# Kernel optimization log

Hardware: AMD Instinct MI355X
Metric: run time of the kernel (lower is better)

## Reference

```python
import jax, jax.numpy as jnp
import numpy as np

B, DIM, HEADS, HW = 32, 384, 8, 48
CH = DIM // HEADS  # 48 channels per head


def pool_matrix(H, s):
    # PyTorch AdaptiveAvgPool2d binning: start=floor(i*H/s), end=ceil((i+1)*H/s)
    P = np.zeros((s, H), np.float32)
    for i in range(s):
        a = (i * H) // s
        b = -((-(i + 1) * H) // s)
        P[i, a:b] = 1.0 / (b - a)
    return jnp.asarray(P)


def dwconv(x, w, b, p):
    # depthwise conv, NCHW, kernel [C,1,k,k], stride 1, symmetric pad p
    y = jax.lax.conv_general_dilated(
        x, w, (1, 1), [(p, p), (p, p)],
        dimension_numbers=('NCHW', 'OIHW', 'NCHW'),
        feature_group_count=x.shape[1])
    if b is not None:
        y = y + b[None, :, None, None]
    return y


def setup_inputs() -> dict:
    key = jax.random.key(0)
    ks = jax.random.split(key, 10)
    s = 0.02
    return {
        'x': jax.random.normal(ks[0], (B, DIM, HW, HW), jnp.float32),
        'ln_w': jnp.ones((DIM,), jnp.float32),
        'ln_b': jnp.zeros((DIM,), jnp.float32),
        'w_qkv': jax.random.normal(ks[1], (3 * DIM, DIM), jnp.float32) * s,
        'w_dw': jax.random.normal(ks[2], (3 * DIM, 1, 3, 3), jnp.float32) * s,
        'temperature': jnp.ones((HEADS, 1, 1), jnp.float32),
        'conv3_w': jax.random.normal(ks[3], (3 * CH, 1, 3, 3), jnp.float32) * s,
        'conv3_b': jnp.zeros((3 * CH,), jnp.float32),
        'conv5_w': jax.random.normal(ks[4], (3 * CH, 1, 5, 5), jnp.float32) * s,
        'conv5_b': jnp.zeros((3 * CH,), jnp.float32),
        'conv7_w': jax.random.normal(ks[5], (2 * CH, 1, 7, 7), jnp.float32) * s,
        'conv7_b': jnp.zeros((2 * CH,), jnp.float32),
        'w_proj': jax.random.normal(ks[6], (DIM, DIM), jnp.float32) * s,
    }


def reference(x, ln_w, ln_b, w_qkv, w_dw, temperature,
              conv3_w, conv3_b, conv5_w, conv5_b, conv7_w, conv7_b, w_proj):
    b, C, H, W = x.shape
    heads, Ch = HEADS, C // HEADS
    N = H * W
    # WithBias LayerNorm over channel dim (biased variance, eps 1e-5)
    mu = x.mean(axis=1, keepdims=True)
    var = ((x - mu) ** 2).mean(axis=1, keepdims=True)
    xn = (x - mu) / jnp.sqrt(var + 1e-5) * ln_w[None, :, None, None] + ln_b[None, :, None, None]
    # qkv: 1x1 conv then depthwise 3x3 (groups = 3*dim)
    qkv = jnp.einsum('bchw,oc->bohw', xn, w_qkv)
    qkv = dwconv(qkv, w_dw, None, 1)
    q, k, v = jnp.split(qkv, 3, axis=1)
    q = q.reshape(b, heads, Ch, N)
    k = k.reshape(b, heads, Ch, N)
    v = v.reshape(b, heads, Ch, N)
    # L2-normalize along token dim (F.normalize eps=1e-12)
    qn = q / jnp.maximum(jnp.linalg.norm(q, axis=-1, keepdims=True), 1e-12)
    kn = k / jnp.maximum(jnp.linalg.norm(k, axis=-1, keepdims=True), 1e-12)
    # channel attention [b,h,Ch,Ch]
    attn = jax.nn.relu(jnp.einsum('bhcn,bhdn->bhcd', qn, kn) * temperature[None])
    # ---- FilterModule (crpe) ----
    v_img = v.reshape(b, heads * Ch, H, W)
    # low-pass: 4 equal channel chunks, adaptive avg pool to (1,3,5,7), bilinear up
    chunk = (heads * Ch) // 4
    lp_parts = []
    for idx, sz in enumerate((1, 3, 5, 7)):
        part = v_img[:, idx * chunk:(idx + 1) * chunk]
        Pr = pool_matrix(H, sz)
        Pc = pool_matrix(W, sz)
        pooled = jnp.einsum('ph,bchw,qw->bcpq', Pr, part, Pc)
        lp_parts.append(jax.image.resize(pooled, (b, chunk, H, W), method='linear'))
    LP = jax.nn.relu(jnp.concatenate(lp_parts, axis=1))
    # high-pass: grouped depthwise convs on [3Ch, 3Ch, 2Ch] channel splits
    s0, s1 = 3 * Ch, 3 * Ch
    HP = jnp.concatenate([
        dwconv(v_img[:, :s0], conv3_w, conv3_b, 1),
        dwconv(v_img[:, s0:s0 + s1], conv5_w, conv5_b, 2),
        dwconv(v_img[:, s0 + s1:], conv7_w, conv7_b, 3),
    ], axis=1)
    HP = HP.reshape(b, heads, Ch, N)
    LPf = LP.reshape(b, heads, Ch, N)
    crpe = qn * HP + LPf
    # ---- output ----
    out = jnp.einsum('bhcd,bhdn->bhcn', attn, v)
    out = (Ch ** -0.5) * out + crpe
    out = out.reshape(b, C, H, W)
    out = jnp.einsum('bchw,oc->bohw', out, w_proj)
    return out
```

## Files before the change

kernel.cpp:

```cpp
#include <hip/hip_runtime.h>

typedef unsigned short u16;
typedef short sh4 __attribute__((ext_vector_type(4)));
typedef short short8 __attribute__((ext_vector_type(8)));
typedef u16 ush8 __attribute__((ext_vector_type(8)));
typedef __bf16 bf16x8 __attribute__((ext_vector_type(8)));
typedef float f32x4 __attribute__((ext_vector_type(4)));

#define NB 32
#define CDIM 384
#define NSP 2304
#define QCH 1152

__device__ __forceinline__ float b2f(u16 u) {
    union { unsigned i; float f; } v; v.i = ((unsigned)u) << 16; return v.f;
}
__device__ __forceinline__ u16 f2b(float f) {
    union { float f; unsigned i; } v; v.f = f;
    unsigned r = v.i + 0x7FFFu + ((v.i >> 16) & 1u);
    return (u16)(r >> 16);
}

__global__ __launch_bounds__(256) void k_prep(const float* __restrict__ wqkv,
                                              const float* __restrict__ wproj,
                                              u16* __restrict__ wqkv_bf,
                                              u16* __restrict__ wproj_bf) {
    int i = blockIdx.x * 256 + threadIdx.x;
    if (i < QCH * CDIM) wqkv_bf[i] = f2b(wqkv[i]);
    if (i < CDIM * CDIM) wproj_bf[i] = f2b(wproj[i]);
}

__global__ __launch_bounds__(256) void k_ln(const float* __restrict__ x,
                                            const float* __restrict__ lnw,
                                            const float* __restrict__ lnb,
                                            u16* __restrict__ xnt) {
    __shared__ float s_sum[4][64], s_sq[4][64], s_mu[64], s_rs[64];
    __shared__ u16 s_tile[64][392];
    int b = blockIdx.y, n0 = blockIdx.x * 64;
    int tid = threadIdx.x, c4 = tid >> 6, nl = tid & 63;
    int cbase = c4 * 96;
    const float* xb = x + (size_t)b * CDIM * NSP + (size_t)cbase * NSP + n0 + nl;
    float v[96];
    float sum = 0.f, sq = 0.f;
#pragma unroll
    for (int j = 0; j < 96; j++) {
        v[j] = xb[(size_t)j * NSP];
        sum += v[j]; sq += v[j] * v[j];
    }
    s_sum[c4][nl] = sum; s_sq[c4][nl] = sq;
    __syncthreads();
    if (tid < 64) {
        float s = s_sum[0][tid] + s_sum[1][tid] + s_sum[2][tid] + s_sum[3][tid];
        float q = s_sq[0][tid] + s_sq[1][tid] + s_sq[2][tid] + s_sq[3][tid];
        float mu = s * (1.f / CDIM);
        float var = q * (1.f / CDIM) - mu * mu;
        s_mu[tid] = mu; s_rs[tid] = rsqrtf(var + 1e-5f);
    }
    __syncthreads();
    float mu = s_mu[nl], rs = s_rs[nl];
#pragma unroll
    for (int j = 0; j < 96; j++) {
        int c = cbase + j;
        s_tile[nl][c] = f2b((v[j] - mu) * rs * lnw[c] + lnb[c]);
    }
    __syncthreads();
    u16* o = xnt + ((size_t)b * NSP + n0) * CDIM;
    for (int i = tid; i < 64 * 48; i += 256) {
        int row = i / 48, c8 = i % 48;
        *(short8*)(o + row * CDIM + c8 * 8) = *(const short8*)(&s_tile[row][c8 * 8]);
    }
}

__global__ __launch_bounds__(256) void k_gemm(const u16* __restrict__ A,
                                              const u16* __restrict__ Bt,
                                              void* __restrict__ Cmat, int M, int f32out) {
    __shared__ u16 As[128][40], Bs[128][40];
    int tid = threadIdx.x;
    int bxn = blockIdx.x, bym = blockIdx.y, bz = blockIdx.z;
    int wave = tid >> 6, lane = tid & 63, wr = wave >> 1, wc = wave & 1;
    int lr = lane & 15, lk = lane >> 4;
    f32x4 acc[4][4];
#pragma unroll
    for (int m = 0; m < 4; m++)
#pragma unroll
        for (int n = 0; n < 4; n++) acc[m][n] = (f32x4){0.f, 0.f, 0.f, 0.f};
    int rs = tid >> 2, ks = (tid & 3) * 8;
    const u16* Ap0 = A + (size_t)(bym * 128 + rs) * 384 + ks;
    const u16* Ap1 = Ap0 + (size_t)64 * 384;
    const u16* Bp0 = Bt + ((size_t)bz * NSP + bxn * 128 + rs) * 384 + ks;
    const u16* Bp1 = Bp0 + (size_t)64 * 384;
    for (int k0 = 0; k0 < 384; k0 += 32) {
        *(short8*)(&As[rs][ks])      = *(const short8*)(Ap0 + k0);
        *(short8*)(&As[rs + 64][ks]) = *(const short8*)(Ap1 + k0);
        *(short8*)(&Bs[rs][ks])      = *(const short8*)(Bp0 + k0);
        *(short8*)(&Bs[rs + 64][ks]) = *(const short8*)(Bp1 + k0);
        __syncthreads();
        short8 af[4], bfr[4];
#pragma unroll
        for (int m = 0; m < 4; m++) af[m] = *(const short8*)(&As[wr * 64 + m * 16 + lr][lk * 8]);
#pragma unroll
        for (int n = 0; n < 4; n++) bfr[n] = *(const short8*)(&Bs[wc * 64 + n * 16 + lr][lk * 8]);
#pragma unroll
        for (int m = 0; m < 4; m++)
#pragma unroll
            for (int n = 0; n < 4; n++)
                acc[m][n] = __builtin_amdgcn_mfma_f32_16x16x32_bf16(
                    __builtin_bit_cast(bf16x8, af[m]), __builtin_bit_cast(bf16x8, bfr[n]),
                    acc[m][n], 0, 0, 0);
        __syncthreads();
    }
#pragma unroll
    for (int m = 0; m < 4; m++)
#pragma unroll
        for (int n = 0; n < 4; n++) {
            int row = bym * 128 + wr * 64 + m * 16 + lk * 4;
            int col = bxn * 128 + wc * 64 + n * 16 + lr;
            if (f32out) {
                float* cp = (float*)Cmat + ((size_t)bz * M + row) * NSP + col;
#pragma unroll
                for (int r = 0; r < 4; r++) cp[(size_t)r * NSP] = acc[m][n][r];
            } else {
                u16* cp = (u16*)Cmat + ((size_t)bz * M + row) * NSP + col;
#pragma unroll
                for (int r = 0; r < 4; r++) cp[(size_t)r * NSP] = f2b(acc[m][n][r]);
            }
        }
}

__global__ __launch_bounds__(192) void k_dw3(u16* __restrict__ qkv,
                                             const float* __restrict__ wdw,
                                             float* __restrict__ sumsq) {
    __shared__ u16 s_in[4 * 2304];
    __shared__ float s_part[192];
    int bx = blockIdx.x, b = blockIdx.y, tid = threadIdx.x;
    u16* gbase = qkv + ((size_t)b * QCH + bx * 4) * NSP;
#pragma unroll
    for (int i = 0; i < 6; i++) {
        int c = tid + i * 192;
        *(ush8*)(&s_in[c * 8]) = *(const ush8*)(gbase + c * 8);
    }
    int p = tid / 48, y = tid % 48;
    int ch = bx * 4 + p;
    float w[9];
#pragma unroll
    for (int i = 0; i < 9; i++) w[i] = wdw[ch * 9 + i];
    __syncthreads();
    const u16* L = &s_in[p * 2304];
    ush8 r0[6], r1[6], r2[6];
#pragma unroll
    for (int o = 0; o < 6; o++) {
        r1[o] = *(const ush8*)(L + y * 48 + o * 8);
        if (y > 0)  r0[o] = *(const ush8*)(L + (y - 1) * 48 + o * 8); else r0[o] = 0;
        if (y < 47) r2[o] = *(const ush8*)(L + (y + 1) * 48 + o * 8); else r2[o] = 0;
    }
    float ss = 0.f;
    short8 outv[6];
#pragma unroll
    for (int g = 0; g < 6; g++) {
        float a0[10], a1[10], a2[10];
#pragma unroll
        for (int j = 0; j < 10; j++) {
            int xi = g * 8 - 1 + j;
            if (xi < 0 || xi >= 48) { a0[j] = 0.f; a1[j] = 0.f; a2[j] = 0.f; }
            else {
                a0[j] = b2f(r0[xi >> 3][xi & 7]);
                a1[j] = b2f(r1[xi >> 3][xi & 7]);
                a2[j] = b2f(r2[xi >> 3][xi & 7]);
            }
        }
        union { u16 u[8]; short8 v; } pk;
#pragma unroll
        for (int x = 0; x < 8; x++) {
            float o = a0[x] * w[0] + a0[x + 1] * w[1] + a0[x + 2] * w[2]
                    + a1[x] * w[3] + a1[x + 1] * w[4] + a1[x + 2] * w[5]
                    + a2[x] * w[6] + a2[x + 1] * w[7] + a2[x + 2] * w[8];
            ss += o * o;
            pk.u[x] = f2b(o);
        }
        outv[g] = pk.v;
    }
    s_part[tid] = ss;
    __syncthreads();
#pragma unroll
    for (int g = 0; g < 6; g++)
        *(short8*)(&s_in[p * 2304 + y * 48 + g * 8]) = outv[g];
    __syncthreads();
#pragma unroll
    for (int i = 0; i < 6; i++) {
        int c = tid + i * 192;
        *(ush8*)(gbase + c * 8) = *(const ush8*)(&s_in[c * 8]);
    }
    if (bx < 192 && tid < 4) {
        float s = 0.f;
        for (int i = 0; i < 48; i++) s += s_part[tid * 48 + i];
        sumsq[b * 768 + bx * 4 + tid] = s;
    }
}

__global__ void k_rnorm(const float* __restrict__ ss, float* __restrict__ rn) {
    int i = blockIdx.x * 256 + threadIdx.x;
    if (i < NB * 768) rn[i] = 1.f / fmaxf(sqrtf(ss[i]), 1e-12f);
}

__global__ __launch_bounds__(512) void k_attn(const u16* __restrict__ qkv,
                                              const float* __restrict__ rn,
                                              const float* __restrict__ temp,
                                              u16* __restrict__ attn) {
    __shared__ float s_part[8][48 * 48];
    int h = blockIdx.x, b = blockIdx.y, tid = threadIdx.x;
    int wave = tid >> 6, lane = tid & 63;
    int lr = lane & 15, lk = lane >> 4;
    const u16* qp = qkv + ((size_t)b * QCH + h * 48) * NSP;
    const u16* kp = qkv + ((size_t)b * QCH + 384 + h * 48) * NSP;
    f32x4 acc[3][3];
#pragma unroll
    for (int m = 0; m < 3; m++)
#pragma unroll
        for (int n = 0; n < 3; n++) acc[m][n] = (f32x4){0.f, 0.f, 0.f, 0.f};
    int k0 = wave * 288 + lk * 8;
    short8 af[3], bf[3], afn[3], bfn[3];
#pragma unroll
    for (int m = 0; m < 3; m++) {
        af[m] = *(const short8*)(qp + (size_t)(m * 16 + lr) * NSP + k0);
        bf[m] = *(const short8*)(kp + (size_t)(m * 16 + lr) * NSP + k0);
    }
    for (int s = 0; s < 9; s++) {
        if (s < 8) {
#pragma unroll
            for (int m = 0; m < 3; m++) {
                afn[m] = *(const short8*)(qp + (size_t)(m * 16 + lr) * NSP + k0 + 32 * (s + 1));
                bfn[m] = *(const short8*)(kp + (size_t)(m * 16 + lr) * NSP + k0 + 32 * (s + 1));
            }
        }
#pragma unroll
        for (int m = 0; m < 3; m++)
#pragma unroll
            for (int n = 0; n < 3; n++)
                acc[m][n] = __builtin_amdgcn_mfma_f32_16x16x32_bf16(
                    __builtin_bit_cast(bf16x8, af[m]), __builtin_bit_cast(bf16x8, bf[n]),
                    acc[m][n], 0, 0, 0);
#pragma unroll
        for (int m = 0; m < 3; m++) { af[m] = afn[m]; bf[m] = bfn[m]; }
    }
#pragma unroll
    for (int m = 0; m < 3; m++)
#pragma unroll
        for (int n = 0; n < 3; n++)
#pragma unroll
            for (int r = 0; r < 4; r++)
                s_part[wave][(m * 16 + lk * 4 + r) * 48 + n * 16 + lr] = acc[m][n][r];
    __syncthreads();
    float th = temp[h];
    const float* rq = rn + b * 768 + h * 48;
    const float* rk = rn + b * 768 + 384 + h * 48;
    u16* ap = attn + ((size_t)(b * 8 + h)) * NSP;
    for (int f = tid; f < 2304; f += 512) {
        int c = f / 48, d = f % 48;
        float v = 0.f;
#pragma unroll
        for (int wv = 0; wv < 8; wv++) v += s_part[wv][f];
        v *= th * rq[c] * rk[d];
        ap[f] = f2b(fmaxf(v, 0.f));
    }
}

template<int KS, int CH0, int NCH>
__global__ __launch_bounds__(256) void k_hp_t(const u16* __restrict__ qkv,
                                              const float* __restrict__ wk,
                                              const float* __restrict__ bk,
                                              u16* __restrict__ hp) {
    constexpr int PAD = KS / 2;
    constexpr int NIN = 8 + 2 * PAD;
    int t = blockIdx.x * 256 + threadIdx.x;
    int y = t % 48;
    int rem = t / 48;
    int chl = rem % NCH;
    int b = rem / NCH;
    int ch = CH0 + chl;
    const u16* src = qkv + ((size_t)b * QCH + 768 + ch) * NSP;
    float bias = bk[chl];
    float acc[48];
#pragma unroll
    for (int i = 0; i < 48; i++) acc[i] = bias;
    for (int dy = 0; dy < KS; dy++) {
        int yy = y - PAD + dy;
        if (yy < 0 || yy >= 48) continue;
        ush8 r[6];
#pragma unroll
        for (int o = 0; o < 6; o++) r[o] = *(const ush8*)(src + yy * 48 + o * 8);
        float wr[KS];
#pragma unroll
        for (int dx = 0; dx < KS; dx++) wr[dx] = wk[chl * KS * KS + dy * KS + dx];
#pragma unroll
        for (int g = 0; g < 6; g++) {
            float a[NIN];
#pragma unroll
            for (int j = 0; j < NIN; j++) {
                int xi = g * 8 - PAD + j;
                a[j] = (xi < 0 || xi >= 48) ? 0.f : b2f(r[xi >> 3][xi & 7]);
            }
#pragma unroll
            for (int x = 0; x < 8; x++) {
                float s = 0.f;
#pragma unroll
                for (int dx = 0; dx < KS; dx++) s += a[x + dx] * wr[dx];
                acc[g * 8 + x] += s;
            }
        }
    }
    u16* dst = hp + ((size_t)b * CDIM + ch) * NSP + y * 48;
#pragma unroll
    for (int g = 0; g < 6; g++) {
        union { u16 u[8]; short8 v; } pk;
#pragma unroll
        for (int x = 0; x < 8; x++) pk.u[x] = f2b(acc[g * 8 + x]);
        *(short8*)(dst + g * 8) = pk.v;
    }
}

__global__ __launch_bounds__(64) void k_pool(const u16* __restrict__ qkv,
                                             float* __restrict__ pooled) {
    int c = blockIdx.x, b = blockIdx.y, tid = threadIdx.x;
    int s = 2 * (c / 96) + 1;
    __shared__ u16 s_p[2304];
    __shared__ float rp[48][7];
    const u16* src = qkv + ((size_t)b * QCH + 768 + c) * NSP;
    for (int f = tid; f < 288; f += 64)
        *(ush8*)(&s_p[f * 8]) = *(const ush8*)(src + f * 8);
    __syncthreads();
    if (tid < 48) {
        for (int q = 0; q < s; q++) {
            int a = q * 48 / s, e = ((q + 1) * 48 + s - 1) / s;
            float sum = 0.f;
            for (int xx = a; xx < e; xx++) sum += b2f(s_p[tid * 48 + xx]);
            rp[tid][q] = sum / (float)(e - a);
        }
    }
    __syncthreads();
    if (tid < s * s) {
        int p = tid / s, q = tid % s;
        int a = p * 48 / s, e = ((p + 1) * 48 + s - 1) / s;
        float sum = 0.f;
        for (int r = a; r < e; r++) sum += rp[r][q];
        pooled[((size_t)b * CDIM + c) * 49 + tid] = sum / (float)(e - a);
    }
}

__global__ __launch_bounds__(256) void k_out(const u16* __restrict__ qkv,
                                             const u16* __restrict__ attn,
                                             const float* __restrict__ rn,
                                             const u16* __restrict__ hp,
                                             const float* __restrict__ pooled,
                                             u16* __restrict__ tmpt) {
    int nc = blockIdx.x, h = blockIdx.y, b = blockIdx.z, tid = threadIdx.x;
    __shared__ u16 s_at[48 * 72];
    __shared__ u16 s_vt[64 * 72];
    __shared__ float s_pool[48][49];
    __shared__ float s_rq[48];
    int n0 = nc * 64;
    for (int f = tid; f < 432; f += 256) *(ush8*)(&s_at[f * 8]) = (ush8)0;
    for (int f = tid; f < 576; f += 256) *(ush8*)(&s_vt[f * 8]) = (ush8)0;
    __syncthreads();
    const u16* ag = attn + ((size_t)(b * 8 + h)) * NSP;
    for (int f = tid; f < 288; f += 256) {
        int c = f / 6, j = f % 6;
        *(ush8*)(&s_at[c * 72 + j * 8]) = *(const ush8*)(ag + c * 48 + j * 8);
    }
    const u16* vsrc = qkv + ((size_t)b * QCH + 768 + h * 48) * NSP + n0;
    for (int f = tid; f < 3072; f += 256) {
        int d = f >> 6, nn = f & 63;
        s_vt[nn * 72 + d] = vsrc[(size_t)d * NSP + nn];
    }
    for (int f = tid; f < 48 * 49; f += 256)
        s_pool[f / 49][f % 49] = pooled[((size_t)b * CDIM + h * 48) * 49 + f];
    if (tid < 48) s_rq[tid] = rn[b * 768 + h * 48 + tid];
    __syncthreads();
    int wave = tid >> 6, lane = tid & 63, lr = lane & 15, lk = lane >> 4;
    f32x4 acc[3];
#pragma unroll
    for (int m = 0; m < 3; m++) acc[m] = (f32x4){0.f, 0.f, 0.f, 0.f};
#pragma unroll
    for (int ks = 0; ks < 2; ks++) {
        short8 bfr = *(const short8*)(&s_vt[(wave * 16 + lr) * 72 + ks * 32 + lk * 8]);
#pragma unroll
        for (int m = 0; m < 3; m++) {
            short8 af = *(const short8*)(&s_at[(m * 16 + lr) * 72 + ks * 32 + lk * 8]);
            acc[m] = __builtin_amdgcn_mfma_f32_16x16x32_bf16(
                __builtin_bit_cast(bf16x8, af), __builtin_bit_cast(bf16x8, bfr),
                acc[m], 0, 0, 0);
        }
    }
    int s = 2 * (h / 2) + 1;
    const float inv = 0.14433756729740643f;
    int n = n0 + wave * 16 + lr;
    int y = n / 48, xx = n % 48;
    float syf = (y + 0.5f) * s * (1.f / 48.f) - 0.5f;
    int iy0 = (int)floorf(syf); float fy = syf - (float)iy0;
    int iy1 = min(iy0 + 1, s - 1); iy0 = max(iy0, 0);
    float sxf = (xx + 0.5f) * s * (1.f / 48.f) - 0.5f;
    int ix0 = (int)floorf(sxf); float fx = sxf - (float)ix0;
    int ix1 = min(ix0 + 1, s - 1); ix0 = max(ix0, 0);
    const u16* qp = qkv + ((size_t)b * QCH + h * 48) * NSP + n;
    const u16* hq = hp + ((size_t)b * CDIM + h * 48) * NSP + n;
    u16* tp = tmpt + ((size_t)b * NSP + n) * CDIM + h * 48;
#pragma unroll
    for (int m = 0; m < 3; m++) {
        int cb = m * 16 + lk * 4;
        union { u16 u[4]; sh4 v; } pk;
#pragma unroll
        for (int r = 0; r < 4; r++) {
            int ch = cb + r;
            float qv = b2f(qp[(size_t)ch * NSP]);
            float hv = b2f(hq[(size_t)ch * NSP]);
            const float* P = s_pool[ch];
            float lp = (1.f - fy) * ((1.f - fx) * P[iy0 * s + ix0] + fx * P[iy0 * s + ix1])
                     + fy * ((1.f - fx) * P[iy1 * s + ix0] + fx * P[iy1 * s + ix1]);
            lp = fmaxf(lp, 0.f);
            pk.u[r] = f2b(inv * acc[m][r] + qv * s_rq[ch] * hv + lp);
        }
        *(sh4*)(tp + cb) = pk.v;
    }
}

extern "C" void kernel_launch(void* const* d_in, const int* in_sizes, int n_in,
                              void* d_out, int out_size, void* d_ws, size_t ws_size,
                              hipStream_t stream) {
    const float* x    = (const float*)d_in[0];
    const float* lnw  = (const float*)d_in[1];
    const float* lnb  = (const float*)d_in[2];
    const float* wqkv = (const float*)d_in[3];
    const float* wdw  = (const float*)d_in[4];
    const float* temp = (const float*)d_in[5];
    const float* w3   = (const float*)d_in[6];
    const float* b3   = (const float*)d_in[7];
    const float* w5   = (const float*)d_in[8];
    const float* b5   = (const float*)d_in[9];
    const float* w7   = (const float*)d_in[10];
    const float* b7   = (const float*)d_in[11];
    const float* wproj= (const float*)d_in[12];
    float* out = (float*)d_out;

    char* w = (char*)d_ws;
    const size_t SZ_XNT = (size_t)NB * NSP * CDIM * 2;
    const size_t SZ_QKV = (size_t)NB * QCH * NSP * 2;
    u16* xnt      = (u16*)w;
    u16* qkvb     = (u16*)(w + SZ_XNT);
    u16* hpb      = (u16*)(w + SZ_XNT + SZ_QKV);
    char* tail    = w + SZ_XNT + SZ_QKV + (size_t)NB * CDIM * NSP * 2;
    float* sumsq  = (float*)tail;
    float* rnorm  = sumsq + NB * 768;
    u16*  attnb   = (u16*)(rnorm + NB * 768);
    float* pooled = (float*)(attnb + (size_t)NB * 8 * NSP);
    u16* wqkv_bf  = (u16*)(pooled + (size_t)NB * CDIM * 49);
    u16* wproj_bf = wqkv_bf + (size_t)QCH * CDIM;
    u16* tmpt = xnt;

    k_prep <<<dim3((QCH * CDIM + 255) / 256), 256, 0, stream>>>(wqkv, wproj, wqkv_bf, wproj_bf);
    k_ln   <<<dim3(36, NB), 256, 0, stream>>>(x, lnw, lnb, xnt);
    k_gemm <<<dim3(18, 9, NB), 256, 0, stream>>>(wqkv_bf, xnt, qkvb, QCH, 0);
    k_dw3  <<<dim3(288, NB), 192, 0, stream>>>(qkvb, wdw, sumsq);
    k_rnorm<<<dim3(96), 256, 0, stream>>>(sumsq, rnorm);
    k_attn <<<dim3(8, NB), 512, 0, stream>>>(qkvb, rnorm, temp, attnb);
    k_hp_t<3, 0, 144>   <<<dim3(864), 256, 0, stream>>>(qkvb, w3, b3, hpb);
    k_hp_t<5, 144, 144> <<<dim3(864), 256, 0, stream>>>(qkvb, w5, b5, hpb);
    k_hp_t<7, 288, 96>  <<<dim3(576), 256, 0, stream>>>(qkvb, w7, b7, hpb);
    k_pool <<<dim3(CDIM, NB), 64, 0, stream>>>(qkvb, pooled);
    k_out  <<<dim3(36, 8, NB), 256, 0, stream>>>(qkvb, attnb, rnorm, hpb, pooled, tmpt);
    k_gemm <<<dim3(18, 3, NB), 256, 0, stream>>>(wproj_bf, tmpt, out, CDIM, 1);
}
```

Baseline: 466.7 us.

## Load GEMM tiles via direct global-to-LDS loads with XOR swizzle and BK=64

```diff
diff --git a/kernel.cpp b/kernel.cpp
--- a/kernel.cpp
+++ b/kernel.cpp
@@ -19,6 +19,10 @@
     union { float f; unsigned i; } v; v.f = f;
     unsigned r = v.i + 0x7FFFu + ((v.i >> 16) & 1u);
     return (u16)(r >> 16);
+}
+__device__ __forceinline__ void gload16(const u16* g, u16* l) {
+    __builtin_amdgcn_global_load_lds((const __attribute__((address_space(1))) unsigned int*)(g),
+                                     (__attribute__((address_space(3))) unsigned int*)(l), 16, 0, 0);
 }
 
 __global__ __launch_bounds__(256) void k_prep(const float* __restrict__ wqkv,
@@ -74,7 +78,8 @@
 __global__ __launch_bounds__(256) void k_gemm(const u16* __restrict__ A,
                                               const u16* __restrict__ Bt,
                                               void* __restrict__ Cmat, int M, int f32out) {
-    __shared__ u16 As[128][40], Bs[128][40];
+    __shared__ __align__(16) u16 As[128 * 64];
+    __shared__ __align__(16) u16 Bs[128 * 64];
     int tid = threadIdx.x;
     int bxn = blockIdx.x, bym = blockIdx.y, bz = blockIdx.z;
     int wave = tid >> 6, lane = tid & 63, wr = wave >> 1, wc = wave & 1;
@@ -84,29 +89,42 @@
     for (int m = 0; m < 4; m++)
 #pragma unroll
         for (int n = 0; n < 4; n++) acc[m][n] = (f32x4){0.f, 0.f, 0.f, 0.f};
-    int rs = tid >> 2, ks = (tid & 3) * 8;
-    const u16* Ap0 = A + (size_t)(bym * 128 + rs) * 384 + ks;
-    const u16* Ap1 = Ap0 + (size_t)64 * 384;
-    const u16* Bp0 = Bt + ((size_t)bz * NSP + bxn * 128 + rs) * 384 + ks;
-    const u16* Bp1 = Bp0 + (size_t)64 * 384;
-    for (int k0 = 0; k0 < 384; k0 += 32) {
-        *(short8*)(&As[rs][ks])      = *(const short8*)(Ap0 + k0);
-        *(short8*)(&As[rs + 64][ks]) = *(const short8*)(Ap1 + k0);
-        *(short8*)(&Bs[rs][ks])      = *(const short8*)(Bp0 + k0);
-        *(short8*)(&Bs[rs + 64][ks]) = *(const short8*)(Bp1 + k0);
+    int coloff = ((lane & 7) ^ (lane >> 3)) * 8;
+    int rsub = lane >> 3;
+    const u16* Ag = A + (size_t)(bym * 128 + wave * 32 + rsub) * 384 + coloff;
+    const u16* Bg = Bt + ((size_t)bz * NSP + bxn * 128 + wave * 32 + rsub) * 384 + coloff;
+    u16* Al = As + (wave * 4) * 512;
+    u16* Bl = Bs + (wave * 4) * 512;
+    for (int k0 = 0; k0 < 384; k0 += 64) {
+#pragma unroll
+        for (int i = 0; i < 4; i++) {
+            gload16(Ag + (size_t)(i * 8) * 384 + k0, Al + i * 512);
+            gload16(Bg + (size_t)(i * 8) * 384 + k0, Bl + i * 512);
+        }
         __syncthreads();
-        short8 af[4], bfr[4];
-#pragma unroll
-        for (int m = 0; m < 4; m++) af[m] = *(const short8*)(&As[wr * 64 + m * 16 + lr][lk * 8]);
-#pragma unroll
-        for (int n = 0; n < 4; n++) bfr[n] = *(const short8*)(&Bs[wc * 64 + n * 16 + lr][lk * 8]);
-#pragma unroll
-        for (int m = 0; m < 4; m++)
-#pragma unroll
-            for (int n = 0; n < 4; n++)
+        short8 bfr[4][2];
+#pragma unroll
+        for (int n = 0; n < 4; n++) {
+            int row = wc * 64 + n * 16 + lr;
+#pragma unroll
+            for (int h = 0; h < 2; h++)
+                bfr[n][h] = *(const short8*)(Bs + row * 64 + ((h * 4 + lk) ^ (lr & 7)) * 8);
+        }
+#pragma unroll
+        for (int m = 0; m < 4; m++) {
+            int row = wr * 64 + m * 16 + lr;
+            short8 a0 = *(const short8*)(As + row * 64 + ((lk) ^ (lr & 7)) * 8);
+            short8 a1 = *(const short8*)(As + row * 64 + ((4 + lk) ^ (lr & 7)) * 8);
+#pragma unroll
+            for (int n = 0; n < 4; n++) {
                 acc[m][n] = __builtin_amdgcn_mfma_f32_16x16x32_bf16(
-                    __builtin_bit_cast(bf16x8, af[m]), __builtin_bit_cast(bf16x8, bfr[n]),
+                    __builtin_bit_cast(bf16x8, a0), __builtin_bit_cast(bf16x8, bfr[n][0]),
                     acc[m][n], 0, 0, 0);
+                acc[m][n] = __builtin_amdgcn_mfma_f32_16x16x32_bf16(
+                    __builtin_bit_cast(bf16x8, a1), __builtin_bit_cast(bf16x8, bfr[n][1]),
+                    acc[m][n], 0, 0, 0);
+            }
+        }
         __syncthreads();
     }
 #pragma unroll
```

After: 460.3 us. About the same (-1.4%).
